# Performance work log

Hardware: AMD Instinct MI355X
Metric: run time of the kernel (lower is better)

Reference implementation:

```python
import jax, jax.numpy as jnp
import numpy as np

N_NODES = 50000
N_EDGES = 800000
IN_CH, HID_CH, OUT_CH = 128, 128, 40


def _glorot(key, fan_in, fan_out):
    lim = jnp.sqrt(6.0 / (fan_in + fan_out))
    return jax.random.uniform(key, (fan_in, fan_out), jnp.float32, -lim, lim)


def setup_inputs() -> dict:
    key = jax.random.key(0)
    ks = jax.random.split(key, 5)
    x = jax.random.normal(ks[0], (N_NODES, IN_CH), jnp.float32)
    edge_index = jax.random.randint(ks[1], (2, N_EDGES), 0, N_NODES, dtype=jnp.int32)
    return {
        "x": x,
        "edge_index": edge_index,
        "W1": _glorot(ks[2], IN_CH, HID_CH),
        "b1": jnp.zeros((HID_CH,), jnp.float32),
        "W2": _glorot(ks[3], HID_CH, HID_CH),
        "b2": jnp.zeros((HID_CH,), jnp.float32),
        "W3": _glorot(ks[4], HID_CH, OUT_CH),
        "b3": jnp.zeros((OUT_CH,), jnp.float32),
    }


def reference(x, edge_index, W1, b1, W2, b2, W3, b3):
    # Dropout is inference-mode identity (training=False). GCNConv (PyG default):
    # add self-loops, symmetric normalization D^-1/2 A_hat D^-1/2, linear + bias.
    n = x.shape[0]
    loop = jnp.arange(n, dtype=edge_index.dtype)
    src = jnp.concatenate([edge_index[0], loop])  # message sources
    dst = jnp.concatenate([edge_index[1], loop])  # aggregation targets
    deg = jax.ops.segment_sum(jnp.ones_like(src, dtype=x.dtype), dst, num_segments=n)
    dinv = jnp.where(deg > 0, deg ** -0.5, 0.0)
    norm = dinv[src] * dinv[dst]  # [E+N], identical across layers

    def conv(h, W, b):
        h = h @ W                                   # [N, F_out]
        msg = h[src] * norm[:, None]                # gather + scale: [E+N, F_out]
        return jax.ops.segment_sum(msg, dst, num_segments=n) + b

    h = jax.nn.relu(conv(x, W1, b1))
    h = jax.nn.relu(conv(h, W2, b2))
    h = conv(h, W3, b3)
    return jax.nn.log_softmax(h, axis=1)
```

## Files before the change

### kernel.cpp

```cpp
#include <hip/hip_runtime.h>
#include <math.h>


typedef short s8v __attribute__((ext_vector_type(8)));
typedef float f4v __attribute__((ext_vector_type(4)));
typedef unsigned short u16;

#define CSR_CAP 64

__device__ inline unsigned short f2b(float f) {
  unsigned int u = __float_as_uint(f);
  return (unsigned short)((u + 0x7fffu + ((u >> 16) & 1u)) >> 16);
}
__device__ inline float b2f(unsigned short b) {
  return __uint_as_float(((unsigned int)b) << 16);
}
__device__ inline f4v mfma16(s8v a, s8v b, f4v c) {
  return __builtin_amdgcn_mfma_f32_16x16x32_bf16(a, b, c, 0, 0, 0);
}

__device__ inline void pack_w_elem(const float* __restrict__ W,
                                   short* __restrict__ Wp, int FOUT_real,
                                   int NCT, int idx) {
  const int j = idx & 7;
  const int lane = (idx >> 3) & 63;
  const int fct = idx >> 9;
  const int ks = fct / NCT, ct = fct - ks * NCT;
  const int k = ks * 32 + (lane >> 4) * 8 + j;
  const int c = ct * 16 + (lane & 15);
  const float v = (c < FOUT_real) ? W[k * FOUT_real + c] : 0.f;
  Wp[idx] = (short)f2b(v);
}

__global__ __launch_bounds__(256) void k_soup(
    const float* __restrict__ x, const float* __restrict__ W1,
    short* __restrict__ Tb1, int nRowTiles, int gemmNB,
    const int* __restrict__ src, const int* __restrict__ dst,
    int* __restrict__ cnt, u16* __restrict__ col, int e, float inv8n,
    int fillNB, const float* __restrict__ W2, short* __restrict__ Wp2,
    const float* __restrict__ W3, short* __restrict__ Wp3) {
  __shared__ short Ws[4 * 8 * 64 * 8];
  const int bid = blockIdx.x;
  const int tid = threadIdx.x;

  if (bid < gemmNB) {
    const float4* w4 = (const float4*)W1;
    for (int it = 0; it < 16; ++it) {
      const int lin4 = it * 256 + tid;
      const int k = lin4 >> 5;
      const float4 v = w4[lin4];
      const int cb = (lin4 & 31) * 4;
      const int ks = k >> 5, kr = k & 31;
      const int laneBase = (kr >> 3) << 4;
      const int j = kr & 7;
      const float fv[4] = {v.x, v.y, v.z, v.w};
#pragma unroll
      for (int q = 0; q < 4; ++q) {
        const int c = cb + q;
        Ws[((ks * 8 + (c >> 4)) * 64 + (laneBase | (c & 15))) * 8 + j] =
            (short)f2b(fv[q]);
      }
    }
    __syncthreads();
    const int wid = tid >> 6, lane = tid & 63;
    const int rowTile = bid * 4 + wid;
    if (rowTile >= nRowTiles) return;
    const int row0 = rowTile * 16;
    const int arow = row0 + (lane & 15);
    const int kcol = (lane >> 4) * 8;
    f4v acc[8];
#pragma unroll
    for (int ct = 0; ct < 8; ++ct) acc[ct] = (f4v)(0.f);
    const float* ap = x + (size_t)arow * 128 + kcol;
#pragma unroll
    for (int ks = 0; ks < 4; ++ks) {
      const float4 a0 = *(const float4*)(ap + ks * 32);
      const float4 a1 = *(const float4*)(ap + ks * 32 + 4);
      s8v af;
      af[0] = (short)f2b(a0.x); af[1] = (short)f2b(a0.y);
      af[2] = (short)f2b(a0.z); af[3] = (short)f2b(a0.w);
      af[4] = (short)f2b(a1.x); af[5] = (short)f2b(a1.y);
      af[6] = (short)f2b(a1.z); af[7] = (short)f2b(a1.w);
#pragma unroll
      for (int ct = 0; ct < 8; ++ct) {
        const s8v bf = *(const s8v*)(Ws + ((ks * 8 + ct) * 64 + lane) * 8);
        acc[ct] = mfma16(af, bf, acc[ct]);
      }
    }
    const int crow0 = row0 + (lane >> 4) * 4;
    const int ccol = lane & 15;
#pragma unroll
    for (int r = 0; r < 4; ++r) {
      short* orow = Tb1 + (size_t)(crow0 + r) * 128 + ccol;
#pragma unroll
      for (int ct = 0; ct < 8; ++ct) orow[ct * 16] = (short)f2b(acc[ct][r]);
    }
  } else if (bid < gemmNB + fillNB) {
    const int fb = bid - gemmNB;
    const int bin = fb & 7;
    const int scanB = fb >> 3;
    const int stride = (fillNB >> 3) * 256;
    for (int i = scanB * 256 + tid; i < e; i += stride) {
      const int d = dst[i];
      int b = (int)((float)d * inv8n);
      b = b > 7 ? 7 : b;
      if (b == bin) {
        const int idx = atomicAdd(&cnt[d], 1);
        col[(size_t)d * CSR_CAP + idx] = (u16)src[i];
      }
    }
  } else {
    int pb = bid - gemmNB - fillNB;
    if (pb < 64) {
      pack_w_elem(W2, Wp2, 128, 8, pb * 256 + tid);
    } else {
      const int idx = (pb - 64) * 256 + tid;
      if (idx < 128 * 48) pack_w_elem(W3, Wp3, 40, 3, idx);
    }
  }
}

template <int FOUT>
__global__ __launch_bounds__(256) void k_aggemm(const short* __restrict__ Tb,
                                                const int* __restrict__ cnt,
                                                const u16* __restrict__ col,
                                                const float* __restrict__ bias,
                                                const short* __restrict__ Wp,
                                                short* __restrict__ Tout, int n) {
  __shared__ short Ht[32 * 128];
  const int tid = threadIdx.x;
  const int base = blockIdx.x * 32;

#pragma unroll
  for (int pass = 0; pass < 2; ++pass) {
    const int nl = pass * 16 + (tid >> 4);
    const int node = base + nl;
    const int c8 = tid & 15;
    const int c0 = c8 * 8;
    float r[8];
#pragma unroll
    for (int j = 0; j < 8; ++j) r[j] = 0.f;
    if (node < n) {
      const int cn = cnt[node];
      const float dn = rsqrtf((float)(cn + 1));
      float acc[8];
      {
        const s8v v = *(const s8v*)(Tb + (size_t)node * 128 + c0);
#pragma unroll
        for (int j = 0; j < 8; ++j) acc[j] = dn * b2f((unsigned short)v[j]);
      }
      const u16* cp = col + (size_t)node * CSR_CAP;
      for (int k = 0; k < cn; ++k) {
        const int s = cp[k];
        const float ds = rsqrtf((float)(cnt[s] + 1));
        const s8v v = *(const s8v*)(Tb + (size_t)s * 128 + c0);
#pragma unroll
        for (int j = 0; j < 8; ++j) acc[j] += ds * b2f((unsigned short)v[j]);
      }
#pragma unroll
      for (int j = 0; j < 8; ++j)
        r[j] = fmaxf(acc[j] * dn + bias[c0 + j], 0.f);
    }
    s8v o;
#pragma unroll
    for (int j = 0; j < 8; ++j) o[j] = (short)f2b(r[j]);
    *(s8v*)((char*)Ht + nl * 256 + ((c0 * 2) ^ ((nl & 7) << 4))) = o;
  }
  __syncthreads();

  constexpr int NCT = FOUT / 16;
  const int wid = tid >> 6, lane = tid & 63;
  const int tile = wid >> 1;
  int ct0, nct;
  if (FOUT == 128) { ct0 = (wid & 1) * 4; nct = 4; }
  else { ct0 = 0; nct = (wid & 1) ? 0 : NCT; }
  if (nct > 0) {
    f4v acc[4];
#pragma unroll
    for (int j = 0; j < 4; ++j) acc[j] = (f4v)(0.f);
    const int lrow = tile * 16 + (lane & 15);
    const int kbase = (lane >> 4) * 8;
#pragma unroll
    for (int ks = 0; ks < 4; ++ks) {
      const int kcol = kbase + ks * 32;
      const s8v af = *(const s8v*)((const char*)Ht + lrow * 256 +
                                   ((kcol * 2) ^ ((lrow & 7) << 4)));
#pragma unroll
      for (int j = 0; j < 4; ++j) {
        if (j < nct) {
          const s8v bf =
              *(const s8v*)(Wp + ((ks * NCT + ct0 + j) * 64 + lane) * 8);
          acc[j] = mfma16(af, bf, acc[j]);
        }
      }
    }
    const int crow0 = base + tile * 16 + (lane >> 4) * 4;
    const int ccol = lane & 15;
#pragma unroll
    for (int r = 0; r < 4; ++r) {
      short* orow = Tout + (size_t)(crow0 + r) * FOUT + ccol;
#pragma unroll
      for (int j = 0; j < 4; ++j)
        if (j < nct) orow[(ct0 + j) * 16] = (short)f2b(acc[j][r]);
    }
  }
}

__global__ __launch_bounds__(256) void k_agg3_lsm(const short* __restrict__ Tb,
                                                  const int* __restrict__ cnt,
                                                  const u16* __restrict__ col,
                                                  const float* __restrict__ bias,
                                                  float* __restrict__ out, int n) {
  const int gtid = blockIdx.x * 256 + threadIdx.x;
  const int node = gtid >> 3;
  const int c8 = gtid & 7;
  if (node >= n) return;
  const int c0 = c8 * 8;
  const bool valid = c8 < 5;
  const int cn = cnt[node];
  const float dn = rsqrtf((float)(cn + 1));
  float acc[8];
#pragma unroll
  for (int j = 0; j < 8; ++j) acc[j] = 0.f;
  if (valid) {
    const s8v v = *(const s8v*)(Tb + (size_t)node * 48 + c0);
#pragma unroll
    for (int j = 0; j < 8; ++j) acc[j] = dn * b2f((unsigned short)v[j]);
  }
  const u16* cp = col + (size_t)node * CSR_CAP;
  for (int k = 0; k < cn; ++k) {
    const int s = cp[k];
    if (valid) {
      const float ds = rsqrtf((float)(cnt[s] + 1));
      const s8v v = *(const s8v*)(Tb + (size_t)s * 48 + c0);
#pragma unroll
      for (int j = 0; j < 8; ++j) acc[j] += ds * b2f((unsigned short)v[j]);
    }
  }
  float r[8];
  float m = -INFINITY;
#pragma unroll
  for (int j = 0; j < 8; ++j) {
    r[j] = valid ? (acc[j] * dn + bias[c0 + j]) : -INFINITY;
    m = fmaxf(m, r[j]);
  }
#pragma unroll
  for (int w = 1; w < 8; w <<= 1) m = fmaxf(m, __shfl_xor(m, w, 64));
  float s = 0.f;
#pragma unroll
  for (int j = 0; j < 8; ++j) s += expf(r[j] - m);
#pragma unroll
  for (int w = 1; w < 8; w <<= 1) s += __shfl_xor(s, w, 64);
  const float ls = logf(s);
  if (valid) {
    float* op = out + (size_t)node * 40 + c0;
    *(float4*)op = make_float4(r[0] - m - ls, r[1] - m - ls, r[2] - m - ls,
                               r[3] - m - ls);
    *(float4*)(op + 4) = make_float4(r[4] - m - ls, r[5] - m - ls,
                                     r[6] - m - ls, r[7] - m - ls);
  }
}

extern "C" void kernel_launch(void* const* d_in, const int* in_sizes, int n_in,
                              void* d_out, int out_size, void* d_ws,
                              size_t ws_size, hipStream_t stream) {
  const float* x  = (const float*)d_in[0];
  const int*   ei = (const int*)d_in[1];
  const float* W1 = (const float*)d_in[2];
  const float* b1 = (const float*)d_in[3];
  const float* W2 = (const float*)d_in[4];
  const float* b2 = (const float*)d_in[5];
  const float* W3 = (const float*)d_in[6];
  const float* b3 = (const float*)d_in[7];
  float* out = (float*)d_out;

  const int n = in_sizes[0] / 128;
  const int e = in_sizes[1] / 2;
  const int* src = ei;
  const int* dst = ei + e;

  char* ws = (char*)d_ws;
  size_t off = 0;
  auto carve = [&](size_t bytes) -> void* {
    void* p = ws + off;
    off = (off + bytes + 255) & ~(size_t)255;
    return p;
  };
  const int nb32 = (n + 31) / 32;
  const size_t rows_pad = (size_t)nb32 * 32;
  int*   cnt = (int*)carve((size_t)n * 4);
  u16*   col = (u16*)carve((size_t)n * CSR_CAP * 2);
  short* A   = (short*)carve(rows_pad * 128 * 2);
  short* B   = (short*)carve(rows_pad * 128 * 2);
  short* Wp2 = (short*)carve(128 * 128 * 2);
  short* Wp3 = (short*)carve(128 * 48 * 2);

  const int nRowTiles = (n + 15) / 16;
  const int gemmNB = (nRowTiles + 3) / 4;
  const int fillNB = 2048;
  const int soupNB = gemmNB + fillNB + 64 + 24;

  hipMemsetAsync(cnt, 0, (size_t)n * 4, stream);
  k_soup<<<soupNB, 256, 0, stream>>>(x, W1, B, nRowTiles, gemmNB, src, dst,
                                     cnt, col, e, 8.0f / (float)n, fillNB,
                                     W2, Wp2, W3, Wp3);
  k_aggemm<128><<<nb32, 256, 0, stream>>>(B, cnt, col, b1, Wp2, A, n);
  k_aggemm<48><<<nb32, 256, 0, stream>>>(A, cnt, col, b2, Wp3, B, n);
  k_agg3_lsm<<<((size_t)n * 8 + 255) / 256, 256, 0, stream>>>(B, cnt, col, b3,
                                                              out, n);
}
```

Measured before the change: 240.5 us.

## Split hidden features into column slices for cache-friendly gather aggregation

Stores the 128-wide bf16 hidden activations as four 32-column slices, each a contiguous array, and aggregates one slice at a time so the gathered working set (50k rows × 64 B) fits better in cache. The aggregate+GEMM kernel now handles 128 nodes per 512-thread block, with each thread covering 8 columns of one slice and walking the neighbour list four times. CSR column writes become nontemporal stores. In exchange, index and degree lookups repeat per slice, blocks are larger (fewer per CU), and the slice order relies on the whole device moving through slices in step, which is not guaranteed.

```diff
diff --git a/kernel.cpp b/kernel.cpp
--- a/kernel.cpp
+++ b/kernel.cpp
@@ -34,7 +34,7 @@
 
 __global__ __launch_bounds__(256) void k_soup(
     const float* __restrict__ x, const float* __restrict__ W1,
-    short* __restrict__ Tb1, int nRowTiles, int gemmNB,
+    short* __restrict__ Tb1, size_t SS, int nRowTiles, int gemmNB,
     const int* __restrict__ src, const int* __restrict__ dst,
     int* __restrict__ cnt, u16* __restrict__ col, int e, float inv8n,
     int fillNB, const float* __restrict__ W2, short* __restrict__ Wp2,
@@ -91,9 +91,10 @@
     const int ccol = lane & 15;
 #pragma unroll
     for (int r = 0; r < 4; ++r) {
-      short* orow = Tb1 + (size_t)(crow0 + r) * 128 + ccol;
-#pragma unroll
-      for (int ct = 0; ct < 8; ++ct) orow[ct * 16] = (short)f2b(acc[ct][r]);
+      short* orow = Tb1 + (size_t)(crow0 + r) * 32 + ccol;
+#pragma unroll
+      for (int ct = 0; ct < 8; ++ct)
+        orow[(size_t)(ct >> 1) * SS + (ct & 1) * 16] = (short)f2b(acc[ct][r]);
     }
   } else if (bid < gemmNB + fillNB) {
     const int fb = bid - gemmNB;
@@ -106,7 +107,7 @@
       b = b > 7 ? 7 : b;
       if (b == bin) {
         const int idx = atomicAdd(&cnt[d], 1);
-        col[(size_t)d * CSR_CAP + idx] = (u16)src[i];
+        __builtin_nontemporal_store((u16)src[i], &col[(size_t)d * CSR_CAP + idx]);
       }
     }
   } else {
@@ -121,87 +122,83 @@
 }
 
 template <int FOUT>
-__global__ __launch_bounds__(256) void k_aggemm(const short* __restrict__ Tb,
-                                                const int* __restrict__ cnt,
-                                                const u16* __restrict__ col,
-                                                const float* __restrict__ bias,
-                                                const short* __restrict__ Wp,
-                                                short* __restrict__ Tout, int n) {
-  __shared__ short Ht[32 * 128];
+__global__ __launch_bounds__(512) void k_aggemm_s(
+    const short* __restrict__ Tsl, const int* __restrict__ cnt,
+    const u16* __restrict__ col, const float* __restrict__ bias,
+    const short* __restrict__ Wp, short* __restrict__ Tout, size_t SS, int n) {
+  __shared__ short Ht[128 * 128];
   const int tid = threadIdx.x;
-  const int base = blockIdx.x * 32;
-
-#pragma unroll
-  for (int pass = 0; pass < 2; ++pass) {
-    const int nl = pass * 16 + (tid >> 4);
-    const int node = base + nl;
-    const int c8 = tid & 15;
-    const int c0 = c8 * 8;
-    float r[8];
-#pragma unroll
-    for (int j = 0; j < 8; ++j) r[j] = 0.f;
+  const int base = blockIdx.x * 128;
+
+  const int nl = tid >> 2;
+  const int node = base + nl;
+  const int c0 = (tid & 3) * 8;
+  int cn = 0;
+  float dn = 0.f;
+  const u16* cp = col + (size_t)node * CSR_CAP;
+  if (node < n) {
+    cn = cnt[node];
+    dn = rsqrtf((float)(cn + 1));
+  }
+#pragma unroll
+  for (int sl = 0; sl < 4; ++sl) {
+    const short* Ts = Tsl + (size_t)sl * SS;
+    float acc[8];
+#pragma unroll
+    for (int j = 0; j < 8; ++j) acc[j] = 0.f;
     if (node < n) {
-      const int cn = cnt[node];
-      const float dn = rsqrtf((float)(cn + 1));
-      float acc[8];
-      {
-        const s8v v = *(const s8v*)(Tb + (size_t)node * 128 + c0);
-#pragma unroll
-        for (int j = 0; j < 8; ++j) acc[j] = dn * b2f((unsigned short)v[j]);
-      }
-      const u16* cp = col + (size_t)node * CSR_CAP;
+      const s8v v = *(const s8v*)(Ts + (size_t)node * 32 + c0);
+#pragma unroll
+      for (int j = 0; j < 8; ++j) acc[j] = dn * b2f((unsigned short)v[j]);
       for (int k = 0; k < cn; ++k) {
         const int s = cp[k];
         const float ds = rsqrtf((float)(cnt[s] + 1));
-        const s8v v = *(const s8v*)(Tb + (size_t)s * 128 + c0);
-#pragma unroll
-        for (int j = 0; j < 8; ++j) acc[j] += ds * b2f((unsigned short)v[j]);
+        const s8v v2 = *(const s8v*)(Ts + (size_t)s * 32 + c0);
+#pragma unroll
+        for (int j = 0; j < 8; ++j) acc[j] += ds * b2f((unsigned short)v2[j]);
       }
-#pragma unroll
-      for (int j = 0; j < 8; ++j)
-        r[j] = fmaxf(acc[j] * dn + bias[c0 + j], 0.f);
-    }
+    }
+    const int cc = sl * 32 + c0;
     s8v o;
 #pragma unroll
-    for (int j = 0; j < 8; ++j) o[j] = (short)f2b(r[j]);
-    *(s8v*)((char*)Ht + nl * 256 + ((c0 * 2) ^ ((nl & 7) << 4))) = o;
+    for (int j = 0; j < 8; ++j) {
+      const float r = (node < n) ? fmaxf(acc[j] * dn + bias[cc + j], 0.f) : 0.f;
+      o[j] = (short)f2b(r);
+    }
+    *(s8v*)((char*)Ht + nl * 256 + ((cc * 2) ^ ((nl & 7) << 4))) = o;
   }
   __syncthreads();
 
   constexpr int NCT = FOUT / 16;
   const int wid = tid >> 6, lane = tid & 63;
-  const int tile = wid >> 1;
-  int ct0, nct;
-  if (FOUT == 128) { ct0 = (wid & 1) * 4; nct = 4; }
-  else { ct0 = 0; nct = (wid & 1) ? 0 : NCT; }
-  if (nct > 0) {
-    f4v acc[4];
-#pragma unroll
-    for (int j = 0; j < 4; ++j) acc[j] = (f4v)(0.f);
-    const int lrow = tile * 16 + (lane & 15);
-    const int kbase = (lane >> 4) * 8;
-#pragma unroll
-    for (int ks = 0; ks < 4; ++ks) {
-      const int kcol = kbase + ks * 32;
-      const s8v af = *(const s8v*)((const char*)Ht + lrow * 256 +
-                                   ((kcol * 2) ^ ((lrow & 7) << 4)));
-#pragma unroll
-      for (int j = 0; j < 4; ++j) {
-        if (j < nct) {
-          const s8v bf =
-              *(const s8v*)(Wp + ((ks * NCT + ct0 + j) * 64 + lane) * 8);
-          acc[j] = mfma16(af, bf, acc[j]);
-        }
-      }
-    }
-    const int crow0 = base + tile * 16 + (lane >> 4) * 4;
-    const int ccol = lane & 15;
-#pragma unroll
-    for (int r = 0; r < 4; ++r) {
-      short* orow = Tout + (size_t)(crow0 + r) * FOUT + ccol;
-#pragma unroll
-      for (int j = 0; j < 4; ++j)
-        if (j < nct) orow[(ct0 + j) * 16] = (short)f2b(acc[j][r]);
+  const int lrow = wid * 16 + (lane & 15);
+  const int kbase = (lane >> 4) * 8;
+  f4v acc[NCT];
+#pragma unroll
+  for (int j = 0; j < NCT; ++j) acc[j] = (f4v)(0.f);
+#pragma unroll
+  for (int ks = 0; ks < 4; ++ks) {
+    const int kcol = ks * 32 + kbase;
+    const s8v af = *(const s8v*)((const char*)Ht + lrow * 256 +
+                                 ((kcol * 2) ^ ((lrow & 7) << 4)));
+#pragma unroll
+    for (int j = 0; j < NCT; ++j) {
+      const s8v bf = *(const s8v*)(Wp + ((ks * NCT + j) * 64 + lane) * 8);
+      acc[j] = mfma16(af, bf, acc[j]);
+    }
+  }
+  const int crow0 = base + wid * 16 + (lane >> 4) * 4;
+  const int ccol = lane & 15;
+#pragma unroll
+  for (int r = 0; r < 4; ++r) {
+#pragma unroll
+    for (int j = 0; j < NCT; ++j) {
+      const short v = (short)f2b(acc[j][r]);
+      if (FOUT == 128)
+        Tout[(size_t)(j >> 1) * SS + (size_t)(crow0 + r) * 32 + (j & 1) * 16 +
+             ccol] = v;
+      else
+        Tout[(size_t)(crow0 + r) * FOUT + j * 16 + ccol] = v;
     }
   }
 }
@@ -286,12 +283,14 @@
     off = (off + bytes + 255) & ~(size_t)255;
     return p;
   };
-  const int nb32 = (n + 31) / 32;
-  const size_t rows_pad = (size_t)nb32 * 32;
+  const int nb128 = (n + 127) / 128;
+  const size_t rows_pad = (size_t)nb128 * 128;
+  const size_t SS = rows_pad * 32;
+
   int*   cnt = (int*)carve((size_t)n * 4);
   u16*   col = (u16*)carve((size_t)n * CSR_CAP * 2);
-  short* A   = (short*)carve(rows_pad * 128 * 2);
-  short* B   = (short*)carve(rows_pad * 128 * 2);
+  short* A   = (short*)carve(4 * SS * 2);
+  short* B   = (short*)carve(4 * SS * 2);
   short* Wp2 = (short*)carve(128 * 128 * 2);
   short* Wp3 = (short*)carve(128 * 48 * 2);
 
@@ -301,11 +300,11 @@
   const int soupNB = gemmNB + fillNB + 64 + 24;
 
   hipMemsetAsync(cnt, 0, (size_t)n * 4, stream);
-  k_soup<<<soupNB, 256, 0, stream>>>(x, W1, B, nRowTiles, gemmNB, src, dst,
+  k_soup<<<soupNB, 256, 0, stream>>>(x, W1, B, SS, nRowTiles, gemmNB, src, dst,
                                      cnt, col, e, 8.0f / (float)n, fillNB,
                                      W2, Wp2, W3, Wp3);
-  k_aggemm<128><<<nb32, 256, 0, stream>>>(B, cnt, col, b1, Wp2, A, n);
-  k_aggemm<48><<<nb32, 256, 0, stream>>>(A, cnt, col, b2, Wp3, B, n);
+  k_aggemm_s<128><<<nb128, 512, 0, stream>>>(B, cnt, col, b1, Wp2, A, SS, n);
+  k_aggemm_s<48><<<nb128, 512, 0, stream>>>(A, cnt, col, b2, Wp3, B, SS, n);
   k_agg3_lsm<<<((size_t)n * 8 + 255) / 256, 256, 0, stream>>>(B, cnt, col, b3,
                                                               out, n);
 }
```

Measured after the change: 339.1 us. +41.0%, slower.

## Precompute inverse-sqrt degrees and fold source scaling into GEMM epilogue

Applied to the files above, without the earlier changes.

Adds a small kernel that precomputes D^-1/2 per node into a buffer. The aggregation+GEMM kernels now scale their output rows by the node's dinv, so the next layer's gather no longer needs the per-neighbour cnt lookup and rsqrt. The gather loops are also unrolled by four to issue more independent loads, and CSR column writes use nontemporal stores. The cost is one extra launch and a dinv buffer, and the bf16 rounding now happens after prescaling, which changes numerics slightly.

```diff
diff --git a/kernel.cpp b/kernel.cpp
--- a/kernel.cpp
+++ b/kernel.cpp
@@ -106,7 +106,7 @@
       b = b > 7 ? 7 : b;
       if (b == bin) {
         const int idx = atomicAdd(&cnt[d], 1);
-        col[(size_t)d * CSR_CAP + idx] = (u16)src[i];
+        __builtin_nontemporal_store((u16)src[i], &col[(size_t)d * CSR_CAP + idx]);
       }
     }
   } else {
@@ -120,10 +120,18 @@
   }
 }
 
-template <int FOUT>
+__global__ __launch_bounds__(256) void k_dinvf(const int* __restrict__ cnt,
+                                               float* __restrict__ dnf,
+                                               int n, int rows_pad) {
+  int i = blockIdx.x * 256 + threadIdx.x;
+  if (i < rows_pad) dnf[i] = (i < n) ? rsqrtf((float)(cnt[i] + 1)) : 0.f;
+}
+
+template <int FOUT, bool PRESCALED>
 __global__ __launch_bounds__(256) void k_aggemm(const short* __restrict__ Tb,
                                                 const int* __restrict__ cnt,
                                                 const u16* __restrict__ col,
+                                                const float* __restrict__ dnf,
                                                 const float* __restrict__ bias,
                                                 const short* __restrict__ Wp,
                                                 short* __restrict__ Tout, int n) {
@@ -142,18 +150,41 @@
     for (int j = 0; j < 8; ++j) r[j] = 0.f;
     if (node < n) {
       const int cn = cnt[node];
-      const float dn = rsqrtf((float)(cn + 1));
+      const float dn = dnf[node];
       float acc[8];
       {
         const s8v v = *(const s8v*)(Tb + (size_t)node * 128 + c0);
 #pragma unroll
-        for (int j = 0; j < 8; ++j) acc[j] = dn * b2f((unsigned short)v[j]);
+        for (int j = 0; j < 8; ++j)
+          acc[j] = (PRESCALED ? 1.f : dn) * b2f((unsigned short)v[j]);
       }
       const u16* cp = col + (size_t)node * CSR_CAP;
-      for (int k = 0; k < cn; ++k) {
+      int k = 0;
+      for (; k + 4 <= cn; k += 4) {
+        const int s0 = cp[k], s1 = cp[k + 1], s2 = cp[k + 2], s3 = cp[k + 3];
+        const s8v v0 = *(const s8v*)(Tb + (size_t)s0 * 128 + c0);
+        const s8v v1 = *(const s8v*)(Tb + (size_t)s1 * 128 + c0);
+        const s8v v2 = *(const s8v*)(Tb + (size_t)s2 * 128 + c0);
+        const s8v v3 = *(const s8v*)(Tb + (size_t)s3 * 128 + c0);
+        if (PRESCALED) {
+#pragma unroll
+          for (int j = 0; j < 8; ++j)
+            acc[j] += b2f((unsigned short)v0[j]) + b2f((unsigned short)v1[j]) +
+                      b2f((unsigned short)v2[j]) + b2f((unsigned short)v3[j]);
+        } else {
+          const float d0 = dnf[s0], d1 = dnf[s1], d2 = dnf[s2], d3 = dnf[s3];
+#pragma unroll
+          for (int j = 0; j < 8; ++j)
+            acc[j] += d0 * b2f((unsigned short)v0[j]) +
+                      d1 * b2f((unsigned short)v1[j]) +
+                      d2 * b2f((unsigned short)v2[j]) +
+                      d3 * b2f((unsigned short)v3[j]);
+        }
+      }
+      for (; k < cn; ++k) {
         const int s = cp[k];
-        const float ds = rsqrtf((float)(cnt[s] + 1));
         const s8v v = *(const s8v*)(Tb + (size_t)s * 128 + c0);
+        const float ds = PRESCALED ? 1.f : dnf[s];
 #pragma unroll
         for (int j = 0; j < 8; ++j) acc[j] += ds * b2f((unsigned short)v[j]);
       }
@@ -198,10 +229,11 @@
     const int ccol = lane & 15;
 #pragma unroll
     for (int r = 0; r < 4; ++r) {
+      const float sc = dnf[crow0 + r];
       short* orow = Tout + (size_t)(crow0 + r) * FOUT + ccol;
 #pragma unroll
       for (int j = 0; j < 4; ++j)
-        if (j < nct) orow[(ct0 + j) * 16] = (short)f2b(acc[j][r]);
+        if (j < nct) orow[(ct0 + j) * 16] = (short)f2b(acc[j][r] * sc);
     }
   }
 }
@@ -209,6 +241,7 @@
 __global__ __launch_bounds__(256) void k_agg3_lsm(const short* __restrict__ Tb,
                                                   const int* __restrict__ cnt,
                                                   const u16* __restrict__ col,
+                                                  const float* __restrict__ dnf,
                                                   const float* __restrict__ bias,
                                                   float* __restrict__ out, int n) {
   const int gtid = blockIdx.x * 256 + threadIdx.x;
@@ -218,23 +251,32 @@
   const int c0 = c8 * 8;
   const bool valid = c8 < 5;
   const int cn = cnt[node];
-  const float dn = rsqrtf((float)(cn + 1));
+  const float dn = dnf[node];
   float acc[8];
 #pragma unroll
   for (int j = 0; j < 8; ++j) acc[j] = 0.f;
+  const u16* cp = col + (size_t)node * CSR_CAP;
   if (valid) {
     const s8v v = *(const s8v*)(Tb + (size_t)node * 48 + c0);
 #pragma unroll
-    for (int j = 0; j < 8; ++j) acc[j] = dn * b2f((unsigned short)v[j]);
-  }
-  const u16* cp = col + (size_t)node * CSR_CAP;
-  for (int k = 0; k < cn; ++k) {
-    const int s = cp[k];
-    if (valid) {
-      const float ds = rsqrtf((float)(cnt[s] + 1));
+    for (int j = 0; j < 8; ++j) acc[j] = b2f((unsigned short)v[j]);
+    int k = 0;
+    for (; k + 4 <= cn; k += 4) {
+      const int s0 = cp[k], s1 = cp[k + 1], s2 = cp[k + 2], s3 = cp[k + 3];
+      const s8v v0 = *(const s8v*)(Tb + (size_t)s0 * 48 + c0);
+      const s8v v1 = *(const s8v*)(Tb + (size_t)s1 * 48 + c0);
+      const s8v v2 = *(const s8v*)(Tb + (size_t)s2 * 48 + c0);
+      const s8v v3 = *(const s8v*)(Tb + (size_t)s3 * 48 + c0);
+#pragma unroll
+      for (int j = 0; j < 8; ++j)
+        acc[j] += b2f((unsigned short)v0[j]) + b2f((unsigned short)v1[j]) +
+                  b2f((unsigned short)v2[j]) + b2f((unsigned short)v3[j]);
+    }
+    for (; k < cn; ++k) {
+      const int s = cp[k];
       const s8v v = *(const s8v*)(Tb + (size_t)s * 48 + c0);
 #pragma unroll
-      for (int j = 0; j < 8; ++j) acc[j] += ds * b2f((unsigned short)v[j]);
+      for (int j = 0; j < 8; ++j) acc[j] += b2f((unsigned short)v[j]);
     }
   }
   float r[8];
@@ -287,11 +329,13 @@
     return p;
   };
   const int nb32 = (n + 31) / 32;
-  const size_t rows_pad = (size_t)nb32 * 32;
+  const int rows_pad = nb32 * 32;
+
   int*   cnt = (int*)carve((size_t)n * 4);
+  float* dnf = (float*)carve((size_t)rows_pad * 4);
   u16*   col = (u16*)carve((size_t)n * CSR_CAP * 2);
-  short* A   = (short*)carve(rows_pad * 128 * 2);
-  short* B   = (short*)carve(rows_pad * 128 * 2);
+  short* A   = (short*)carve((size_t)rows_pad * 128 * 2);
+  short* B   = (short*)carve((size_t)rows_pad * 128 * 2);
   short* Wp2 = (short*)carve(128 * 128 * 2);
   short* Wp3 = (short*)carve(128 * 48 * 2);
 
@@ -304,8 +348,9 @@
   k_soup<<<soupNB, 256, 0, stream>>>(x, W1, B, nRowTiles, gemmNB, src, dst,
                                      cnt, col, e, 8.0f / (float)n, fillNB,
                                      W2, Wp2, W3, Wp3);
-  k_aggemm<128><<<nb32, 256, 0, stream>>>(B, cnt, col, b1, Wp2, A, n);
-  k_aggemm<48><<<nb32, 256, 0, stream>>>(A, cnt, col, b2, Wp3, B, n);
-  k_agg3_lsm<<<((size_t)n * 8 + 255) / 256, 256, 0, stream>>>(B, cnt, col, b3,
-                                                              out, n);
-}
+  k_dinvf<<<(rows_pad + 255) / 256, 256, 0, stream>>>(cnt, dnf, n, rows_pad);
+  k_aggemm<128, false><<<nb32, 256, 0, stream>>>(B, cnt, col, dnf, b1, Wp2, A, n);
+  k_aggemm<48, true><<<nb32, 256, 0, stream>>>(A, cnt, col, dnf, b2, Wp3, B, n);
+  k_agg3_lsm<<<((size_t)n * 8 + 255) / 256, 256, 0, stream>>>(B, cnt, col, dnf,
+                                                              b3, out, n);
+}
```

Measured after the change: 221.9 us. 1.08x faster.

## Split neighbor gathers across lanes and prescale GEMM outputs by source degree

Applied to the files above, without the earlier changes.

Aggregation now assigns one wavefront per node, with edge subsets spread across lane groups (4 in the hidden layers, 8 in the final layer), two gathers in flight per lane, and a shuffle reduction at the end. The GEMM epilogue now multiplies each output row by its own dinv, so later layers skip the per-edge degree lookup and rsqrt. The goal is more memory-level parallelism on the irregular gathers and fewer dependent loads per edge. The cost is the shuffle reductions and idle lanes for low-degree nodes; the first layer's k_soup output is still unscaled, so that layer keeps the per-edge scaling path.

```diff
diff --git a/kernel.cpp b/kernel.cpp
--- a/kernel.cpp
+++ b/kernel.cpp
@@ -120,7 +120,7 @@
   }
 }
 
-template <int FOUT>
+template <int FOUT, bool PRESCALED>
 __global__ __launch_bounds__(256) void k_aggemm(const short* __restrict__ Tb,
                                                 const int* __restrict__ cnt,
                                                 const u16* __restrict__ col,
@@ -130,46 +130,77 @@
   __shared__ short Ht[32 * 128];
   const int tid = threadIdx.x;
   const int base = blockIdx.x * 32;
-
-#pragma unroll
-  for (int pass = 0; pass < 2; ++pass) {
-    const int nl = pass * 16 + (tid >> 4);
+  const int wid = tid >> 6, lane = tid & 63;
+  const int es = lane >> 4;
+  const int c8 = lane & 15;
+  const int c0 = c8 * 8;
+
+  for (int iter = 0; iter < 8; ++iter) {
+    const int nl = iter * 4 + wid;
     const int node = base + nl;
-    const int c8 = tid & 15;
-    const int c0 = c8 * 8;
-    float r[8];
-#pragma unroll
-    for (int j = 0; j < 8; ++j) r[j] = 0.f;
     if (node < n) {
       const int cn = cnt[node];
       const float dn = rsqrtf((float)(cn + 1));
       float acc[8];
-      {
+      if (es == 0) {
         const s8v v = *(const s8v*)(Tb + (size_t)node * 128 + c0);
 #pragma unroll
-        for (int j = 0; j < 8; ++j) acc[j] = dn * b2f((unsigned short)v[j]);
+        for (int j = 0; j < 8; ++j)
+          acc[j] = (PRESCALED ? 1.f : dn) * b2f((unsigned short)v[j]);
+      } else {
+#pragma unroll
+        for (int j = 0; j < 8; ++j) acc[j] = 0.f;
       }
       const u16* cp = col + (size_t)node * CSR_CAP;
-      for (int k = 0; k < cn; ++k) {
-        const int s = cp[k];
-        const float ds = rsqrtf((float)(cnt[s] + 1));
-        const s8v v = *(const s8v*)(Tb + (size_t)s * 128 + c0);
-#pragma unroll
-        for (int j = 0; j < 8; ++j) acc[j] += ds * b2f((unsigned short)v[j]);
-      }
-#pragma unroll
-      for (int j = 0; j < 8; ++j)
-        r[j] = fmaxf(acc[j] * dn + bias[c0 + j], 0.f);
-    }
-    s8v o;
-#pragma unroll
-    for (int j = 0; j < 8; ++j) o[j] = (short)f2b(r[j]);
-    *(s8v*)((char*)Ht + nl * 256 + ((c0 * 2) ^ ((nl & 7) << 4))) = o;
+      int k = es;
+      while (k + 4 < cn) {
+        const int s0 = cp[k];
+        const int s1 = cp[k + 4];
+        const s8v v0 = *(const s8v*)(Tb + (size_t)s0 * 128 + c0);
+        const s8v v1 = *(const s8v*)(Tb + (size_t)s1 * 128 + c0);
+        if (PRESCALED) {
+#pragma unroll
+          for (int j = 0; j < 8; ++j)
+            acc[j] += b2f((unsigned short)v0[j]) + b2f((unsigned short)v1[j]);
+        } else {
+          const float d0 = rsqrtf((float)(cnt[s0] + 1));
+          const float d1 = rsqrtf((float)(cnt[s1] + 1));
+#pragma unroll
+          for (int j = 0; j < 8; ++j)
+            acc[j] += d0 * b2f((unsigned short)v0[j]) +
+                      d1 * b2f((unsigned short)v1[j]);
+        }
+        k += 8;
+      }
+      if (k < cn) {
+        const int s0 = cp[k];
+        const s8v v0 = *(const s8v*)(Tb + (size_t)s0 * 128 + c0);
+        const float d0 = PRESCALED ? 1.f : rsqrtf((float)(cnt[s0] + 1));
+#pragma unroll
+        for (int j = 0; j < 8; ++j) acc[j] += d0 * b2f((unsigned short)v0[j]);
+      }
+#pragma unroll
+      for (int j = 0; j < 8; ++j) {
+        acc[j] += __shfl_xor(acc[j], 16, 64);
+        acc[j] += __shfl_xor(acc[j], 32, 64);
+      }
+      if (es == 0) {
+        s8v o;
+#pragma unroll
+        for (int j = 0; j < 8; ++j)
+          o[j] = (short)f2b(fmaxf(acc[j] * dn + bias[c0 + j], 0.f));
+        *(s8v*)((char*)Ht + nl * 256 + ((c0 * 2) ^ ((nl & 7) << 4))) = o;
+      }
+    } else if (es == 0) {
+      s8v o;
+#pragma unroll
+      for (int j = 0; j < 8; ++j) o[j] = 0;
+      *(s8v*)((char*)Ht + nl * 256 + ((c0 * 2) ^ ((nl & 7) << 4))) = o;
+    }
   }
   __syncthreads();
 
   constexpr int NCT = FOUT / 16;
-  const int wid = tid >> 6, lane = tid & 63;
   const int tile = wid >> 1;
   int ct0, nct;
   if (FOUT == 128) { ct0 = (wid & 1) * 4; nct = 4; }
@@ -198,10 +229,12 @@
     const int ccol = lane & 15;
 #pragma unroll
     for (int r = 0; r < 4; ++r) {
-      short* orow = Tout + (size_t)(crow0 + r) * FOUT + ccol;
+      const int row = crow0 + r;
+      const float sc = (row < n) ? rsqrtf((float)(cnt[row] + 1)) : 0.f;
+      short* orow = Tout + (size_t)row * FOUT + ccol;
 #pragma unroll
       for (int j = 0; j < 4; ++j)
-        if (j < nct) orow[(ct0 + j) * 16] = (short)f2b(acc[j][r]);
+        if (j < nct) orow[(ct0 + j) * 16] = (short)f2b(acc[j][r] * sc);
     }
   }
 }
@@ -211,48 +244,65 @@
                                                   const u16* __restrict__ col,
                                                   const float* __restrict__ bias,
                                                   float* __restrict__ out, int n) {
-  const int gtid = blockIdx.x * 256 + threadIdx.x;
-  const int node = gtid >> 3;
-  const int c8 = gtid & 7;
+  const int node = (blockIdx.x * 256 + threadIdx.x) >> 6;
+  const int lane = threadIdx.x & 63;
+  const int es = lane >> 3;
+  const int c8 = lane & 7;
   if (node >= n) return;
   const int c0 = c8 * 8;
-  const bool valid = c8 < 5;
+  const bool gval = c8 < 5;
   const int cn = cnt[node];
   const float dn = rsqrtf((float)(cn + 1));
   float acc[8];
 #pragma unroll
   for (int j = 0; j < 8; ++j) acc[j] = 0.f;
-  if (valid) {
-    const s8v v = *(const s8v*)(Tb + (size_t)node * 48 + c0);
-#pragma unroll
-    for (int j = 0; j < 8; ++j) acc[j] = dn * b2f((unsigned short)v[j]);
-  }
   const u16* cp = col + (size_t)node * CSR_CAP;
-  for (int k = 0; k < cn; ++k) {
-    const int s = cp[k];
-    if (valid) {
-      const float ds = rsqrtf((float)(cnt[s] + 1));
-      const s8v v = *(const s8v*)(Tb + (size_t)s * 48 + c0);
-#pragma unroll
-      for (int j = 0; j < 8; ++j) acc[j] += ds * b2f((unsigned short)v[j]);
-    }
+  if (gval) {
+    if (es == 0) {
+      const s8v v = *(const s8v*)(Tb + (size_t)node * 48 + c0);
+#pragma unroll
+      for (int j = 0; j < 8; ++j) acc[j] = b2f((unsigned short)v[j]);
+    }
+    int k = es;
+    while (k + 8 < cn) {
+      const int s0 = cp[k];
+      const int s1 = cp[k + 8];
+      const s8v v0 = *(const s8v*)(Tb + (size_t)s0 * 48 + c0);
+      const s8v v1 = *(const s8v*)(Tb + (size_t)s1 * 48 + c0);
+#pragma unroll
+      for (int j = 0; j < 8; ++j)
+        acc[j] += b2f((unsigned short)v0[j]) + b2f((unsigned short)v1[j]);
+      k += 16;
+    }
+    if (k < cn) {
+      const int s0 = cp[k];
+      const s8v v0 = *(const s8v*)(Tb + (size_t)s0 * 48 + c0);
+#pragma unroll
+      for (int j = 0; j < 8; ++j) acc[j] += b2f((unsigned short)v0[j]);
+    }
+  }
+#pragma unroll
+  for (int j = 0; j < 8; ++j) {
+    acc[j] += __shfl_xor(acc[j], 8, 64);
+    acc[j] += __shfl_xor(acc[j], 16, 64);
+    acc[j] += __shfl_xor(acc[j], 32, 64);
   }
   float r[8];
   float m = -INFINITY;
 #pragma unroll
   for (int j = 0; j < 8; ++j) {
-    r[j] = valid ? (acc[j] * dn + bias[c0 + j]) : -INFINITY;
+    r[j] = gval ? (acc[j] * dn + bias[c0 + j]) : -INFINITY;
     m = fmaxf(m, r[j]);
   }
 #pragma unroll
   for (int w = 1; w < 8; w <<= 1) m = fmaxf(m, __shfl_xor(m, w, 64));
   float s = 0.f;
 #pragma unroll
-  for (int j = 0; j < 8; ++j) s += expf(r[j] - m);
+  for (int j = 0; j < 8; ++j) s += gval ? expf(r[j] - m) : 0.f;
 #pragma unroll
   for (int w = 1; w < 8; w <<= 1) s += __shfl_xor(s, w, 64);
   const float ls = logf(s);
-  if (valid) {
+  if (es == 0 && gval) {
     float* op = out + (size_t)node * 40 + c0;
     *(float4*)op = make_float4(r[0] - m - ls, r[1] - m - ls, r[2] - m - ls,
                                r[3] - m - ls);
@@ -287,11 +337,12 @@
     return p;
   };
   const int nb32 = (n + 31) / 32;
-  const size_t rows_pad = (size_t)nb32 * 32;
+  const int rows_pad = nb32 * 32;
+
   int*   cnt = (int*)carve((size_t)n * 4);
   u16*   col = (u16*)carve((size_t)n * CSR_CAP * 2);
-  short* A   = (short*)carve(rows_pad * 128 * 2);
-  short* B   = (short*)carve(rows_pad * 128 * 2);
+  short* A   = (short*)carve((size_t)rows_pad * 128 * 2);
+  short* B   = (short*)carve((size_t)rows_pad * 128 * 2);
   short* Wp2 = (short*)carve(128 * 128 * 2);
   short* Wp3 = (short*)carve(128 * 48 * 2);
 
@@ -304,8 +355,8 @@
   k_soup<<<soupNB, 256, 0, stream>>>(x, W1, B, nRowTiles, gemmNB, src, dst,
                                      cnt, col, e, 8.0f / (float)n, fillNB,
                                      W2, Wp2, W3, Wp3);
-  k_aggemm<128><<<nb32, 256, 0, stream>>>(B, cnt, col, b1, Wp2, A, n);
-  k_aggemm<48><<<nb32, 256, 0, stream>>>(A, cnt, col, b2, Wp3, B, n);
-  k_agg3_lsm<<<((size_t)n * 8 + 255) / 256, 256, 0, stream>>>(B, cnt, col, b3,
-                                                              out, n);
-}
+  k_aggemm<128, false><<<nb32, 256, 0, stream>>>(B, cnt, col, b1, Wp2, A, n);
+  k_aggemm<48, true><<<nb32, 256, 0, stream>>>(A, cnt, col, b2, Wp3, B, n);
+  k_agg3_lsm<<<((size_t)n * 64 + 255) / 256, 256, 0, stream>>>(B, cnt, col, b3,
+                                                               out, n);
+}
```

Result: no change. 241.3 us (+0.3%).
